# Optimization experiments

Measured on AMD Instinct MI355X. Metric: run time of the kernel, lower is better.

The kernel has to match this reference:

```python
import jax, jax.numpy as jnp
import numpy as np

RGB_W = (0.2989, 0.587, 0.114)
EPS = 1e-8  # guard only; original divides without eps


def _saliency_map(img):
    """Faithful jax port of SaliencyMap: gray -> uint8 -> cv2.Sobel(ksize=3,
    BORDER_REFLECT_101) -> magnitude -> per-image min-max normalize.
    img: [B, C, H, W] float in [0,1]. Returns [B, 1, H, W] float32.
    """
    B, C, H, W = img.shape
    if C == 3:
        gray = RGB_W[0] * img[:, 0] + RGB_W[1] * img[:, 1] + RGB_W[2] * img[:, 2]
    else:
        gray = img[:, 0]
    # (gray*255).astype(np.uint8): truncating cast, then cv2 promotes to float
    q = (gray * 255.0).astype(jnp.uint8).astype(jnp.float32)  # [B,H,W]
    # cv2 default border: BORDER_REFLECT_101 == jnp.pad mode 'reflect'
    p = jnp.pad(q, ((0, 0), (1, 1), (1, 1)), mode='reflect')  # [B,H+2,W+2]
    # Sobel x (correlation with [[-1,0,1],[-2,0,2],[-1,0,1]])
    gx = (p[:, :-2, 2:] + 2.0 * p[:, 1:-1, 2:] + p[:, 2:, 2:]
          - p[:, :-2, :-2] - 2.0 * p[:, 1:-1, :-2] - p[:, 2:, :-2])
    # Sobel y (transpose kernel)
    gy = (p[:, 2:, :-2] + 2.0 * p[:, 2:, 1:-1] + p[:, 2:, 2:]
          - p[:, :-2, :-2] - 2.0 * p[:, :-2, 1:-1] - p[:, :-2, 2:])
    mag = jnp.sqrt(gx * gx + gy * gy)  # [B,H,W]
    mn = jnp.min(mag, axis=(1, 2), keepdims=True)
    mx = jnp.max(mag, axis=(1, 2), keepdims=True)
    norm = (mag - mn) / jnp.maximum(mx - mn, EPS)  # cv2 NORM_MINMAX to [0,1]
    return norm[:, None]  # [B,1,H,W]


def setup_inputs() -> dict:
    key = jax.random.key(0)
    k1, k2, k3 = jax.random.split(key, 3)
    shape = (16, 3, 512, 512)
    return {
        "img_vis": jax.random.uniform(k1, shape, dtype=jnp.float32),
        "img_ir": jax.random.uniform(k2, shape, dtype=jnp.float32),
        "img_fusion": jax.random.uniform(k3, shape, dtype=jnp.float32),
    }


def reference(img_vis, img_ir, img_fusion):
    s_vis = _saliency_map(img_vis)  # [B,1,H,W]
    s_ir = _saliency_map(img_ir)
    denom = s_vis + s_ir + EPS  # eps guard against 0/0 (see notes)
    w_vis = s_vis / denom
    w_ir = s_ir / denom
    img_sal = w_vis * img_vis + w_ir * img_ir  # broadcasts over channels
    loss = jnp.mean(jnp.abs(img_sal - img_fusion))  # F.l1_loss (mean)
    return loss
```

## Files before the change

### kernel.cpp

```cpp
#include <hip/hip_runtime.h>
#include <hip/hip_bf16.h>
#include <stdint.h>

#define H 512
#define W 512
#define HW (H * W)
#define SR 4
#define NSTRIP (H / SR)

__device__ __forceinline__ int refl(int i, int n) {
    return i < 0 ? -i : (i >= n ? 2 * n - 2 - i : i);
}

__device__ __forceinline__ void graywin(const float4* __restrict__ p4, int y, int lane,
                                        float* __restrict__ h) {
    int o = refl(y, H) * (W / 4) + lane * 2;
    float4 r0 = p4[o],                  r1 = p4[o + 1];
    float4 g0 = p4[o + HW / 4],         g1 = p4[o + 1 + HW / 4];
    float4 b0 = p4[o + 2 * (HW / 4)],   b1 = p4[o + 1 + 2 * (HW / 4)];
    float g[8];
    g[0] = floorf((0.2989f * r0.x + 0.587f * g0.x + 0.114f * b0.x) * 255.0f);
    g[1] = floorf((0.2989f * r0.y + 0.587f * g0.y + 0.114f * b0.y) * 255.0f);
    g[2] = floorf((0.2989f * r0.z + 0.587f * g0.z + 0.114f * b0.z) * 255.0f);
    g[3] = floorf((0.2989f * r0.w + 0.587f * g0.w + 0.114f * b0.w) * 255.0f);
    g[4] = floorf((0.2989f * r1.x + 0.587f * g1.x + 0.114f * b1.x) * 255.0f);
    g[5] = floorf((0.2989f * r1.y + 0.587f * g1.y + 0.114f * b1.y) * 255.0f);
    g[6] = floorf((0.2989f * r1.z + 0.587f * g1.z + 0.114f * b1.z) * 255.0f);
    g[7] = floorf((0.2989f * r1.w + 0.587f * g1.w + 0.114f * b1.w) * 255.0f);
    #pragma unroll
    for (int j = 0; j < 8; ++j) h[j + 1] = g[j];
    float up = __shfl_up(g[7], 1);
    float dn = __shfl_down(g[0], 1);
    h[0] = (lane == 0)  ? g[1] : up;
    h[9] = (lane == 63) ? g[6] : dn;
}

__global__ __launch_bounds__(256) void k_sal(const float* __restrict__ vis,
                                             const float* __restrict__ ir,
                                             uint8_t* __restrict__ qvis,
                                             uint8_t* __restrict__ qir,
                                             float* __restrict__ pm, int B) {
    int lane = threadIdx.x & 63;
    int gwave = blockIdx.x * 4 + (threadIdx.x >> 6);
    int per_src = B * NSTRIP;
    int src = gwave >= per_src;
    int rem = src ? gwave - per_src : gwave;
    int b     = rem >> 7;
    int strip = rem & 127;
    int y0 = strip * SR;

    const float4* p4 = (const float4*)((src ? ir : vis) + (size_t)b * 3 * HW);
    uint8_t* q = (src ? qir : qvis) + (size_t)b * HW;

    float rw[3][10];
    graywin(p4, y0 - 1, lane, rw[0]);
    graywin(p4, y0,     lane, rw[1]);

    float mn = INFINITY, mx = 0.0f;
    #pragma unroll
    for (int r = 0; r < SR; ++r) {
        float* hm = rw[r % 3];
        float* h0 = rw[(r + 1) % 3];
        float* hp = rw[(r + 2) % 3];
        graywin(p4, y0 + r + 1, lane, hp);

        uint32_t u0 = ((uint32_t)h0[1]) | ((uint32_t)h0[2] << 8) |
                      ((uint32_t)h0[3] << 16) | ((uint32_t)h0[4] << 24);
        uint32_t u1 = ((uint32_t)h0[5]) | ((uint32_t)h0[6] << 8) |
                      ((uint32_t)h0[7] << 16) | ((uint32_t)h0[8] << 24);
        uint2 qw; qw.x = u0; qw.y = u1;
        *(uint2*)(q + (size_t)(y0 + r) * W + lane * 8) = qw;

        float sx[10], sy[10];
        #pragma unroll
        for (int j = 0; j < 10; ++j) {
            sx[j] = hm[j] + 2.0f * h0[j] + hp[j];
            sy[j] = hp[j] - hm[j];
        }
        #pragma unroll
        for (int k = 0; k < 8; ++k) {
            float gx = sx[k + 2] - sx[k];
            float gy = sy[k] + 2.0f * sy[k + 1] + sy[k + 2];
            float m = sqrtf(gx * gx + gy * gy);
            mn = fminf(mn, m);
            mx = fmaxf(mx, m);
        }
    }

    #pragma unroll
    for (int o = 32; o > 0; o >>= 1) {
        mn = fminf(mn, __shfl_down(mn, o));
        mx = fmaxf(mx, __shfl_down(mx, o));
    }
    if (lane == 0) {
        float* o = pm + ((size_t)(src * B + b) * NSTRIP + strip) * 2;
        o[0] = mn;
        o[1] = mx;
    }
}

__device__ __forceinline__ void row_cols(uint2 v, int lane, float* __restrict__ c) {
    uint32_t lx = __shfl_up(v.y, 1);
    uint32_t rx = __shfl_down(v.x, 1);
    uint32_t lb = (lane == 0)  ? ((v.x >> 8) & 0xffu)  : (lx >> 24);
    uint32_t rb = (lane == 63) ? ((v.y >> 16) & 0xffu) : (rx & 0xffu);
    c[0] = (float)lb;
    c[1] = (float)(v.x & 0xffu);
    c[2] = (float)((v.x >> 8) & 0xffu);
    c[3] = (float)((v.x >> 16) & 0xffu);
    c[4] = (float)(v.x >> 24);
    c[5] = (float)(v.y & 0xffu);
    c[6] = (float)((v.y >> 8) & 0xffu);
    c[7] = (float)((v.y >> 16) & 0xffu);
    c[8] = (float)(v.y >> 24);
    c[9] = (float)rb;
}

__device__ __forceinline__ void sobel_row8(const uint8_t* __restrict__ q, int y, int lane,
                                           float* __restrict__ mag) {
    const uint2* rm = (const uint2*)(q + (size_t)refl(y - 1, H) * W);
    const uint2* r0 = (const uint2*)(q + (size_t)y * W);
    const uint2* rp = (const uint2*)(q + (size_t)refl(y + 1, H) * W);
    uint2 vm = rm[lane], v0 = r0[lane], vp = rp[lane];
    float c0[10], c1[10], c2[10];
    row_cols(vm, lane, c0);
    row_cols(v0, lane, c1);
    row_cols(vp, lane, c2);
    float sx[10], sy[10];
    #pragma unroll
    for (int j = 0; j < 10; ++j) {
        sx[j] = c0[j] + 2.0f * c1[j] + c2[j];
        sy[j] = c2[j] - c0[j];
    }
    #pragma unroll
    for (int k = 0; k < 8; ++k) {
        float gx = sx[k + 2] - sx[k];
        float gy = sy[k] + 2.0f * sy[k + 1] + sy[k + 2];
        mag[k] = sqrtf(gx * gx + gy * gy);
    }
}

__global__ __launch_bounds__(256) void k_loss(const float* __restrict__ vis,
                                              const float* __restrict__ ir,
                                              const float* __restrict__ fus,
                                              const uint8_t* __restrict__ qvis,
                                              const uint8_t* __restrict__ qir,
                                              const float* __restrict__ pm,
                                              float* __restrict__ partial, int B) {
    int w = threadIdx.x >> 6, lane = threadIdx.x & 63;
    int b = blockIdx.x >> 6;
    int y0 = (blockIdx.x & 63) * 8;

    __shared__ float sred[4];
    {
        int src = w >> 1, qsel = w & 1;
        const float* base = pm + (size_t)(src * B + b) * NSTRIP * 2;
        float v0 = base[lane * 2 + qsel];
        float v1 = base[(lane + 64) * 2 + qsel];
        float v = qsel ? fmaxf(v0, v1) : fminf(v0, v1);
        if (qsel == 0) {
            #pragma unroll
            for (int o = 32; o > 0; o >>= 1) v = fminf(v, __shfl_down(v, o));
        } else {
            #pragma unroll
            for (int o = 32; o > 0; o >>= 1) v = fmaxf(v, __shfl_down(v, o));
        }
        if (lane == 0) sred[w] = v;
    }
    __syncthreads();
    float mn_v = sred[0], mx_v = sred[1], mn_i = sred[2], mx_i = sred[3];
    float inv_v = 1.0f / fmaxf(mx_v - mn_v, 1e-8f);
    float inv_i = 1.0f / fmaxf(mx_i - mn_i, 1e-8f);

    float acc = 0.0f;
    #pragma unroll
    for (int rr = 0; rr < 2; ++rr) {
        int y = y0 + w + rr * 4;
        float mv[8], mi[8];
        sobel_row8(qvis + (size_t)b * HW, y, lane, mv);
        sobel_row8(qir  + (size_t)b * HW, y, lane, mi);

        float wv[8], wi[8];
        #pragma unroll
        for (int k = 0; k < 8; ++k) {
            float sv = (mv[k] - mn_v) * inv_v;
            float si = (mi[k] - mn_i) * inv_i;
            float den = sv + si + 1e-8f;
            float rden = 1.0f / den;
            wv[k] = sv * rden;
            wi[k] = si * rden;
        }

        int i = y * W + lane * 8;
        #pragma unroll
        for (int ch = 0; ch < 3; ++ch) {
            size_t e4 = ((((size_t)b * 3 + ch) * HW) + i) >> 2;
            const float4* v4 = (const float4*)vis;
            const float4* r4 = (const float4*)ir;
            const float4* f4 = (const float4*)fus;
            float4 va = v4[e4], vb = v4[e4 + 1];
            float4 ra = r4[e4], rb = r4[e4 + 1];
            float4 fa = f4[e4], fb = f4[e4 + 1];
            acc += fabsf(wv[0] * va.x + wi[0] * ra.x - fa.x);
            acc += fabsf(wv[1] * va.y + wi[1] * ra.y - fa.y);
            acc += fabsf(wv[2] * va.z + wi[2] * ra.z - fa.z);
            acc += fabsf(wv[3] * va.w + wi[3] * ra.w - fa.w);
            acc += fabsf(wv[4] * vb.x + wi[4] * rb.x - fb.x);
            acc += fabsf(wv[5] * vb.y + wi[5] * rb.y - fb.y);
            acc += fabsf(wv[6] * vb.z + wi[6] * rb.z - fb.z);
            acc += fabsf(wv[7] * vb.w + wi[7] * rb.w - fb.w);
        }
    }

    #pragma unroll
    for (int o = 32; o > 0; o >>= 1) acc += __shfl_down(acc, o);
    __shared__ float ssum[4];
    if (lane == 0) ssum[w] = acc;
    __syncthreads();
    if (threadIdx.x == 0) partial[blockIdx.x] = ssum[0] + ssum[1] + ssum[2] + ssum[3];
}

__global__ void k_final(const float* __restrict__ partial, int n, float* __restrict__ out,
                        long long N) {
    double s = 0.0;
    for (int i = threadIdx.x; i < n; i += 256) s += (double)partial[i];
    __shared__ double sm[256];
    sm[threadIdx.x] = s;
    __syncthreads();
    for (int k = 128; k > 0; k >>= 1) {
        if (threadIdx.x < k) sm[threadIdx.x] += sm[threadIdx.x + k];
        __syncthreads();
    }
    if (threadIdx.x == 0) out[0] = (float)(sm[0] / (double)N);
}

extern "C" void kernel_launch(void* const* d_in, const int* in_sizes, int n_in,
                              void* d_out, int out_size, void* d_ws, size_t ws_size,
                              hipStream_t stream) {
    const float* vis = (const float*)d_in[0];
    const float* ir  = (const float*)d_in[1];
    const float* fus = (const float*)d_in[2];
    int B = in_sizes[0] / (3 * HW);

    uint8_t* qvis = (uint8_t*)d_ws;
    uint8_t* qir  = qvis + (size_t)B * HW;
    float* pm      = (float*)(qir + (size_t)B * HW);
    float* partial = pm + (size_t)2 * B * NSTRIP * 2;
    float* out = (float*)d_out;

    int nblk_sal = 2 * B * NSTRIP / 4;
    k_sal<<<nblk_sal, 256, 0, stream>>>(vis, ir, qvis, qir, pm, B);

    int nblk_loss = B * (H / 8);
    k_loss<<<nblk_loss, 256, 0, stream>>>(vis, ir, fus, qvis, qir, pm, partial, B);

    k_final<<<1, 256, 0, stream>>>(partial, nblk_loss, out, (long long)B * 3 * HW);
}
```

Measured before the change: 58.28 us.

## Split saliency kernel into grayscale quantize pass and uint8 Sobel min/max pass

Replaces the fused gray+Sobel+min/max kernel with two kernels. The first converts RGB to quantized uint8 gray with no halo rows, and the second computes the Sobel magnitude min/max from the uint8 buffer. This removes the fused kernel's redundant float loads of halo rows (6 rows read per 4 output rows) and its serial register pipeline. In exchange it adds a kernel launch and an extra pass over the uint8 gray image, which is small and likely L2-resident.

```diff
diff --git a/kernel.cpp b/kernel.cpp
--- a/kernel.cpp
+++ b/kernel.cpp
@@ -5,98 +5,56 @@
 #define H 512
 #define W 512
 #define HW (H * W)
-#define SR 4
-#define NSTRIP (H / SR)
+#define NSTRIP 128
 
 __device__ __forceinline__ int refl(int i, int n) {
     return i < 0 ? -i : (i >= n ? 2 * n - 2 - i : i);
 }
 
-__device__ __forceinline__ void graywin(const float4* __restrict__ p4, int y, int lane,
-                                        float* __restrict__ h) {
-    int o = refl(y, H) * (W / 4) + lane * 2;
-    float4 r0 = p4[o],                  r1 = p4[o + 1];
-    float4 g0 = p4[o + HW / 4],         g1 = p4[o + 1 + HW / 4];
-    float4 b0 = p4[o + 2 * (HW / 4)],   b1 = p4[o + 1 + 2 * (HW / 4)];
-    float g[8];
-    g[0] = floorf((0.2989f * r0.x + 0.587f * g0.x + 0.114f * b0.x) * 255.0f);
-    g[1] = floorf((0.2989f * r0.y + 0.587f * g0.y + 0.114f * b0.y) * 255.0f);
-    g[2] = floorf((0.2989f * r0.z + 0.587f * g0.z + 0.114f * b0.z) * 255.0f);
-    g[3] = floorf((0.2989f * r0.w + 0.587f * g0.w + 0.114f * b0.w) * 255.0f);
-    g[4] = floorf((0.2989f * r1.x + 0.587f * g1.x + 0.114f * b1.x) * 255.0f);
-    g[5] = floorf((0.2989f * r1.y + 0.587f * g1.y + 0.114f * b1.y) * 255.0f);
-    g[6] = floorf((0.2989f * r1.z + 0.587f * g1.z + 0.114f * b1.z) * 255.0f);
-    g[7] = floorf((0.2989f * r1.w + 0.587f * g1.w + 0.114f * b1.w) * 255.0f);
-    #pragma unroll
-    for (int j = 0; j < 8; ++j) h[j + 1] = g[j];
-    float up = __shfl_up(g[7], 1);
-    float dn = __shfl_down(g[0], 1);
-    h[0] = (lane == 0)  ? g[1] : up;
-    h[9] = (lane == 63) ? g[6] : dn;
-}
-
-__global__ __launch_bounds__(256) void k_sal(const float* __restrict__ vis,
-                                             const float* __restrict__ ir,
-                                             uint8_t* __restrict__ qvis,
-                                             uint8_t* __restrict__ qir,
-                                             float* __restrict__ pm, int B) {
+__device__ __forceinline__ uint2 gray8(float4 ra, float4 rb, float4 ga, float4 gb,
+                                       float4 ba, float4 bb) {
+    uint32_t t0 = (uint32_t)((0.2989f * ra.x + 0.587f * ga.x + 0.114f * ba.x) * 255.0f);
+    uint32_t t1 = (uint32_t)((0.2989f * ra.y + 0.587f * ga.y + 0.114f * ba.y) * 255.0f);
+    uint32_t t2 = (uint32_t)((0.2989f * ra.z + 0.587f * ga.z + 0.114f * ba.z) * 255.0f);
+    uint32_t t3 = (uint32_t)((0.2989f * ra.w + 0.587f * ga.w + 0.114f * ba.w) * 255.0f);
+    uint32_t t4 = (uint32_t)((0.2989f * rb.x + 0.587f * gb.x + 0.114f * bb.x) * 255.0f);
+    uint32_t t5 = (uint32_t)((0.2989f * rb.y + 0.587f * gb.y + 0.114f * bb.y) * 255.0f);
+    uint32_t t6 = (uint32_t)((0.2989f * rb.z + 0.587f * gb.z + 0.114f * bb.z) * 255.0f);
+    uint32_t t7 = (uint32_t)((0.2989f * rb.w + 0.587f * gb.w + 0.114f * bb.w) * 255.0f);
+    uint2 o;
+    o.x = t0 | (t1 << 8) | (t2 << 16) | (t3 << 24);
+    o.y = t4 | (t5 << 8) | (t6 << 16) | (t7 << 24);
+    return o;
+}
+
+__global__ __launch_bounds__(256) void k_gray(const float* __restrict__ vis,
+                                              const float* __restrict__ ir,
+                                              uint8_t* __restrict__ qvis,
+                                              uint8_t* __restrict__ qir, int B) {
     int lane = threadIdx.x & 63;
     int gwave = blockIdx.x * 4 + (threadIdx.x >> 6);
-    int per_src = B * NSTRIP;
+    int per_src = B * 256;
     int src = gwave >= per_src;
     int rem = src ? gwave - per_src : gwave;
-    int b     = rem >> 7;
-    int strip = rem & 127;
-    int y0 = strip * SR;
+    int b  = rem >> 8;
+    int y0 = (rem & 255) * 2;
 
     const float4* p4 = (const float4*)((src ? ir : vis) + (size_t)b * 3 * HW);
     uint8_t* q = (src ? qir : qvis) + (size_t)b * HW;
 
-    float rw[3][10];
-    graywin(p4, y0 - 1, lane, rw[0]);
-    graywin(p4, y0,     lane, rw[1]);
-
-    float mn = INFINITY, mx = 0.0f;
-    #pragma unroll
-    for (int r = 0; r < SR; ++r) {
-        float* hm = rw[r % 3];
-        float* h0 = rw[(r + 1) % 3];
-        float* hp = rw[(r + 2) % 3];
-        graywin(p4, y0 + r + 1, lane, hp);
-
-        uint32_t u0 = ((uint32_t)h0[1]) | ((uint32_t)h0[2] << 8) |
-                      ((uint32_t)h0[3] << 16) | ((uint32_t)h0[4] << 24);
-        uint32_t u1 = ((uint32_t)h0[5]) | ((uint32_t)h0[6] << 8) |
-                      ((uint32_t)h0[7] << 16) | ((uint32_t)h0[8] << 24);
-        uint2 qw; qw.x = u0; qw.y = u1;
-        *(uint2*)(q + (size_t)(y0 + r) * W + lane * 8) = qw;
-
-        float sx[10], sy[10];
-        #pragma unroll
-        for (int j = 0; j < 10; ++j) {
-            sx[j] = hm[j] + 2.0f * h0[j] + hp[j];
-            sy[j] = hp[j] - hm[j];
-        }
-        #pragma unroll
-        for (int k = 0; k < 8; ++k) {
-            float gx = sx[k + 2] - sx[k];
-            float gy = sy[k] + 2.0f * sy[k + 1] + sy[k + 2];
-            float m = sqrtf(gx * gx + gy * gy);
-            mn = fminf(mn, m);
-            mx = fmaxf(mx, m);
-        }
-    }
-
-    #pragma unroll
-    for (int o = 32; o > 0; o >>= 1) {
-        mn = fminf(mn, __shfl_down(mn, o));
-        mx = fmaxf(mx, __shfl_down(mx, o));
-    }
-    if (lane == 0) {
-        float* o = pm + ((size_t)(src * B + b) * NSTRIP + strip) * 2;
-        o[0] = mn;
-        o[1] = mx;
-    }
+    int o0 = y0 * (W / 4) + lane * 2;
+    int o1 = o0 + (W / 4);
+    float4 r0a = p4[o0],                 r0b = p4[o0 + 1];
+    float4 g0a = p4[o0 + HW / 4],        g0b = p4[o0 + 1 + HW / 4];
+    float4 b0a = p4[o0 + 2 * (HW / 4)],  b0b = p4[o0 + 1 + 2 * (HW / 4)];
+    float4 r1a = p4[o1],                 r1b = p4[o1 + 1];
+    float4 g1a = p4[o1 + HW / 4],        g1b = p4[o1 + 1 + HW / 4];
+    float4 b1a = p4[o1 + 2 * (HW / 4)],  b1b = p4[o1 + 1 + 2 * (HW / 4)];
+
+    uint2 q0 = gray8(r0a, r0b, g0a, g0b, b0a, b0b);
+    uint2 q1 = gray8(r1a, r1b, g1a, g1b, b1a, b1b);
+    *(uint2*)(q + (size_t)y0 * W + lane * 8)       = q0;
+    *(uint2*)(q + (size_t)(y0 + 1) * W + lane * 8) = q1;
 }
 
 __device__ __forceinline__ void row_cols(uint2 v, int lane, float* __restrict__ c) {
@@ -137,6 +95,42 @@
         float gx = sx[k + 2] - sx[k];
         float gy = sy[k] + 2.0f * sy[k + 1] + sy[k + 2];
         mag[k] = sqrtf(gx * gx + gy * gy);
+    }
+}
+
+__global__ __launch_bounds__(256) void k_mm(const uint8_t* __restrict__ qvis,
+                                            const uint8_t* __restrict__ qir,
+                                            float* __restrict__ pm, int B) {
+    int lane = threadIdx.x & 63;
+    int gwave = blockIdx.x * 4 + (threadIdx.x >> 6);
+    int per_src = B * NSTRIP;
+    int src = gwave >= per_src;
+    int rem = src ? gwave - per_src : gwave;
+    int b     = rem >> 7;
+    int strip = rem & 127;
+    int y0 = strip * 4;
+    const uint8_t* q = (src ? qir : qvis) + (size_t)b * HW;
+
+    float mn = INFINITY, mx = 0.0f;
+    #pragma unroll
+    for (int r = 0; r < 4; ++r) {
+        float mag[8];
+        sobel_row8(q, y0 + r, lane, mag);
+        #pragma unroll
+        for (int k = 0; k < 8; ++k) {
+            mn = fminf(mn, mag[k]);
+            mx = fmaxf(mx, mag[k]);
+        }
+    }
+    #pragma unroll
+    for (int o = 32; o > 0; o >>= 1) {
+        mn = fminf(mn, __shfl_down(mn, o));
+        mx = fmaxf(mx, __shfl_down(mx, o));
+    }
+    if (lane == 0) {
+        float* o = pm + ((size_t)(src * B + b) * NSTRIP + strip) * 2;
+        o[0] = mn;
+        o[1] = mx;
     }
 }
 
@@ -248,8 +242,11 @@
     float* partial = pm + (size_t)2 * B * NSTRIP * 2;
     float* out = (float*)d_out;
 
-    int nblk_sal = 2 * B * NSTRIP / 4;
-    k_sal<<<nblk_sal, 256, 0, stream>>>(vis, ir, qvis, qir, pm, B);
+    int nblk_gray = 2 * B * 256 / 4;
+    k_gray<<<nblk_gray, 256, 0, stream>>>(vis, ir, qvis, qir, B);
+
+    int nblk_mm = 2 * B * NSTRIP / 4;
+    k_mm<<<nblk_mm, 256, 0, stream>>>(qvis, qir, pm, B);
 
     int nblk_loss = B * (H / 8);
     k_loss<<<nblk_loss, 256, 0, stream>>>(vis, ir, fus, qvis, qir, pm, partial, B);
```

Result: no change. 58.65 us (+0.6%).
